# Kernel optimization log

Hardware: AMD Instinct MI355X
Metric: run time of the kernel (lower is better)

Reference implementation:

```python
import jax, jax.numpy as jnp
import numpy as np

# ---- module hyperparameters (match init_kwargs) ----
N_BASIS = 4            # lagrange polynomial order n
SEGMENTS = 32
IN_CHANNELS = 64
LENGTH = 2.0
HALF = 0.5 * LENGTH
W_WIDTH = (N_BASIS - 1) * SEGMENTS + 1  # 97
# Lagrange interpolation nodes on [-HALF, HALF] (uniform, as in high_order_layers_torch LagrangePoly)
_XNODES = np.linspace(-HALF, HALF, N_BASIS).astype(np.float32)


def _lagrange_basis(x):
    """x: [...] -> basis values [..., n]; basis_j(x) = prod_{m!=j} (x-X_m)/(X_j-X_m)."""
    X = jnp.asarray(_XNODES, dtype=x.dtype)
    eye = jnp.eye(N_BASIS, dtype=bool)
    denom = jnp.where(eye, 1.0, X[:, None] - X[None, :])          # [n, n]
    num = x[..., None, None] - X                                   # [..., 1, n] broadcast over j
    terms = jnp.where(eye, 1.0, num / denom)                       # [..., j, m]
    return jnp.prod(terms, axis=-1)                                # [..., n]


def setup_inputs() -> dict:
    key = jax.random.key(0)
    k1, k2 = jax.random.split(key)
    x = jax.random.normal(k1, (32, IN_CHANNELS, 4096), dtype=jnp.float32)
    w = jax.random.uniform(k2, (IN_CHANNELS, W_WIDTH), dtype=jnp.float32,
                           minval=-1.0, maxval=1.0)
    return {"x": x, "w": w}


def reference(x, w):
    B, C, N = x.shape  # [batch, channels, nodes]
    n = N_BASIS

    # bin index with torch-style trunc + clamp
    id_raw = jnp.trunc((x + HALF) / LENGTH * SEGMENTS).astype(jnp.int32)
    id_min = jnp.clip(id_raw, 0, SEGMENTS - 1)                     # [B, C, N]
    id_max = id_min + 1

    wid_min = id_min * (n - 1)                                     # [B, C, N]

    # gather n consecutive weights per element from the shared table
    E = B * C * N
    wrange = wid_min.reshape(-1)[:, None] + jnp.arange(n)          # [E, n]
    # original: windex = (arange(E*n)//n) % in_channels  == (arange(E) % C) per row
    windex = (jnp.arange(E) % C)[:, None]                          # [E, 1]
    wg = w[windex, wrange]                                         # [E, n]
    # original reshape: view(-1, nodes, in_channels, n)
    wv = wg.reshape(B, N, C, n)                                    # [B, N, C, n]

    # rescale x into the local segment coordinate [-HALF, HALF]
    eta = lambda idx: idx.astype(x.dtype) / SEGMENTS * 2.0 - 1.0
    x_min = eta(id_min)
    x_max = eta(id_max)
    x_in = LENGTH * ((x - x_min) / (x_max - x_min)) - HALF         # [B, C, N]

    basis = _lagrange_basis(x_in)                                  # [B, C, N, n]
    # contract basis with gathered weights (note transposed node/channel layout of wv)
    out = jnp.einsum("bcnj,bncj->bcn", basis, wv)                  # [B, C, N]
    return out
```

## Files before the change

### kernel.cpp

```cpp
#include <hip/hip_runtime.h>

#define NCH      64
#define WW       97
#define NTHREADS 512

typedef float        f32x4  __attribute__((ext_vector_type(4)));
typedef float        f32x4u __attribute__((ext_vector_type(4), aligned(4)));
typedef _Float16     h16x4  __attribute__((ext_vector_type(4)));
typedef _Float16     h16x8  __attribute__((ext_vector_type(8)));
typedef unsigned int u32;
typedef unsigned int u32x2 __attribute__((ext_vector_type(2)));

__global__ __launch_bounds__(NTHREADS)
void pw_kernel(const float* __restrict__ x,
               const float* __restrict__ w,
               float* __restrict__ out) {
  __shared__ h16x4 wexp[NCH * 32];
  __shared__ __align__(8) unsigned char sidT[64 * 72];

  const int g   = blockIdx.x;
  const int b   = (g & 7) | ((g >> 9) << 3);
  const int t   = (g >> 3) & 63;
  const int tid = threadIdx.x;

  const float* xrow = x + (((size_t)(b * NCH + t)) << 12);
  const f32x4 r0 = *reinterpret_cast<const f32x4*>(xrow + (tid << 3));
  const f32x4 r1 = *reinterpret_cast<const f32x4*>(xrow + (tid << 3) + 4);

  #pragma unroll
  for (int k = 0; k < 2; ++k) {
    const int pr = tid + k * NTHREADS;
    const int c  = pr >> 4, k2 = pr & 15;
    const float* wr = w + c * WW + 6 * k2;
    const f32x4u wa = *reinterpret_cast<const f32x4u*>(wr);
    const f32x4u wb = *reinterpret_cast<const f32x4u*>(wr + 3);
    h16x8 hh;
    {
      const float A = wa[3] - wa[0], B = wa[3] + wa[0];
      const float C = wa[1] - wa[2], D = wa[1] + wa[2];
      hh[0] = (_Float16)fmaf(D, 0.5625f, B * -0.0625f);
      hh[1] = (_Float16)fmaf(C, -1.6875f, A * -0.0625f);
      hh[2] = (_Float16)((B - D) * 0.5625f);
      hh[3] = (_Float16)fmaf(C, 1.6875f, A * 0.5625f);
    }
    {
      const float A = wb[3] - wb[0], B = wb[3] + wb[0];
      const float C = wb[1] - wb[2], D = wb[1] + wb[2];
      hh[4] = (_Float16)fmaf(D, 0.5625f, B * -0.0625f);
      hh[5] = (_Float16)fmaf(C, -1.6875f, A * -0.0625f);
      hh[6] = (_Float16)((B - D) * 0.5625f);
      hh[7] = (_Float16)fmaf(C, 1.6875f, A * 0.5625f);
    }
    *reinterpret_cast<h16x8*>(&wexp[(c << 5) + (k2 << 1)]) = hh;
  }

  {
    u32 p0 = 0, p1 = 0;
    #pragma unroll
    for (int i = 0; i < 4; ++i) {
      const float t0 = fmaf(r0[i], 16.0f, 16.0f);
      int id0 = (int)t0;
      id0 = id0 < 0 ? 0 : (id0 > 31 ? 31 : id0);
      p0 |= (u32)id0 << (8 * i);
      const float t1 = fmaf(r1[i], 16.0f, 16.0f);
      int id1 = (int)t1;
      id1 = id1 < 0 ? 0 : (id1 > 31 ? 31 : id1);
      p1 |= (u32)id1 << (8 * i);
    }
    u32x2 pv; pv[0] = p0; pv[1] = p1;
    *reinterpret_cast<u32x2*>(&sidT[(tid >> 3) * 72 + ((tid & 7) << 3)]) = pv;
  }
  __syncthreads();

  const int l  = tid & 63;
  const int wv = tid >> 6;
  const int q  = l & 15;
  const int a  = l >> 4;
  const int u0 = q << 2;
  const int c0 = (wv << 3) + (a << 1);

  const int dwo = (c0 >> 2) << 2;
  u32 idw[4];
  #pragma unroll
  for (int i = 0; i < 4; ++i)
    idw[i] = *reinterpret_cast<const u32*>(&sidT[(u0 + i) * 72 + dwo]);
  const int sh0 = (c0 & 3) * 8;

  const size_t obase = (((size_t)(b * NCH + c0)) << 12) + ((size_t)(t << 6)) + u0;

  #pragma unroll
  for (int j = 0; j < 2; ++j) {
    const f32x4 own = *reinterpret_cast<const f32x4*>(x + obase + ((size_t)j << 12));
    const int cb = (c0 + j) << 5;
    const int sh = sh0 + 8 * j;
    f32x4 res;
    #pragma unroll
    for (int i = 0; i < 4; ++i) {
      const float xv = own[i];
      const float tt = fmaf(xv, 16.0f, 16.0f);
      int idm = (int)tt;
      idm = idm < 0 ? 0 : (idm > 31 ? 31 : idm);
      const float xin = fmaf(xv, 32.0f, fmaf((float)idm, -2.0f, 31.0f));

      const int widx = (idw[i] >> sh) & 31;
      const h16x4 hc = wexp[cb + widx];
      res[i] = fmaf(fmaf(fmaf((float)hc[3], xin, (float)hc[2]), xin,
                         (float)hc[1]), xin, (float)hc[0]);
    }
    __builtin_nontemporal_store(res,
        reinterpret_cast<f32x4*>(out + obase + ((size_t)j << 12)));
  }
}

extern "C" void kernel_launch(void* const* d_in, const int* in_sizes, int n_in,
                              void* d_out, int out_size, void* d_ws, size_t ws_size,
                              hipStream_t stream) {
  const float* x = (const float*)d_in[0];
  const float* w = (const float*)d_in[1];
  float* out    = (float*)d_out;
  pw_kernel<<<dim3(2048), NTHREADS, 0, stream>>>(x, w, out);
}
```

Measured before the change: 16.30 us.

## Tile index transpose as cyclic 16^3 cube orbits so x is read once

Each element's output depends on the bin id of a permuted element (c,t,u) -> (t,u,c) index. The old kernel read each x row twice: once to build the transposed id table and again for its own value. The new scheme splits each batch's 64x64x64 index space into 16-cubes grouped by cyclic rotation orbits. Each block stages up to three cubes whose transposes map onto each other, so every loaded x value is reused for both id staging and its own output. This halves global reads of x, at the cost of more complex indexing, uneven work per block (orbits of size 1 vs 3) and fewer blocks (768).

Result: slower. 22.56 us (+38.4%).

```diff
diff --git a/kernel.cpp b/kernel.cpp
--- a/kernel.cpp
+++ b/kernel.cpp
@@ -1,8 +1,7 @@
 #include <hip/hip_runtime.h>
 
-#define NCH      64
-#define WW       97
-#define NTHREADS 512
+#define NCH 64
+#define WW  97
 
 typedef float        f32x4  __attribute__((ext_vector_type(4)));
 typedef float        f32x4u __attribute__((ext_vector_type(4), aligned(4)));
@@ -11,25 +10,41 @@
 typedef unsigned int u32;
 typedef unsigned int u32x2 __attribute__((ext_vector_type(2)));
 
-__global__ __launch_bounds__(NTHREADS)
+__constant__ unsigned char ORBITS[24] = {
+  0x00, 0x15, 0x2A, 0x3F,
+  0x01, 0x02, 0x03, 0x05, 0x0A, 0x0F,
+  0x06, 0x09, 0x07, 0x0D, 0x0B, 0x0E,
+  0x16, 0x17, 0x1A, 0x1F, 0x2B, 0x2F,
+  0x1B, 0x1E
+};
+
+#define TAU_STR 24
+#define RHO_STR 392
+
+__global__ __launch_bounds__(512)
 void pw_kernel(const float* __restrict__ x,
                const float* __restrict__ w,
                float* __restrict__ out) {
   __shared__ h16x4 wexp[NCH * 32];
-  __shared__ __align__(8) unsigned char sidT[64 * 72];
+  __shared__ __align__(8) unsigned char sid[3][16 * RHO_STR];
 
-  const int g   = blockIdx.x;
-  const int b   = (g & 7) | ((g >> 9) << 3);
-  const int t   = (g >> 3) & 63;
+  const int g    = blockIdx.x;
+  const int b    = g & 31;
+  const int o    = g >> 5;
+  const int ob   = ORBITS[o];
+  const int nreg = (o < 4) ? 1 : 3;
+  const int e0   = ((ob >> 4) & 3) << 4;
+  const int e1   = ((ob >> 2) & 3) << 4;
+  const int e2   = (ob & 3) << 4;
+
   const int tid = threadIdx.x;
-
-  const float* xrow = x + (((size_t)(b * NCH + t)) << 12);
-  const f32x4 r0 = *reinterpret_cast<const f32x4*>(xrow + (tid << 3));
-  const f32x4 r1 = *reinterpret_cast<const f32x4*>(xrow + (tid << 3) + 4);
+  const int rho = tid >> 5;
+  const int sig = (tid >> 1) & 15;
+  const int h   = tid & 1;
 
   #pragma unroll
   for (int k = 0; k < 2; ++k) {
-    const int pr = tid + k * NTHREADS;
+    const int pr = tid + k * 512;
     const int c  = pr >> 4, k2 = pr & 15;
     const float* wr = w + c * WW + 6 * k2;
     const f32x4u wa = *reinterpret_cast<const f32x4u*>(wr);
@@ -54,61 +69,71 @@
     *reinterpret_cast<h16x8*>(&wexp[(c << 5) + (k2 << 1)]) = hh;
   }
 
-  {
+  auto stage = [&](int r, int R, int T, int O, f32x4& qa, f32x4& qb) {
+    const float* p = x + (((size_t)(b * NCH + R + rho)) << 12)
+                       + ((T + sig) << 6) + O + 8 * h;
+    qa = *reinterpret_cast<const f32x4*>(p);
+    qb = *reinterpret_cast<const f32x4*>(p + 4);
     u32 p0 = 0, p1 = 0;
     #pragma unroll
     for (int i = 0; i < 4; ++i) {
-      const float t0 = fmaf(r0[i], 16.0f, 16.0f);
+      const float t0 = fmaf(qa[i], 16.0f, 16.0f);
       int id0 = (int)t0;
       id0 = id0 < 0 ? 0 : (id0 > 31 ? 31 : id0);
       p0 |= (u32)id0 << (8 * i);
-      const float t1 = fmaf(r1[i], 16.0f, 16.0f);
+      const float t1 = fmaf(qb[i], 16.0f, 16.0f);
       int id1 = (int)t1;
       id1 = id1 < 0 ? 0 : (id1 > 31 ? 31 : id1);
       p1 |= (u32)id1 << (8 * i);
     }
     u32x2 pv; pv[0] = p0; pv[1] = p1;
-    *reinterpret_cast<u32x2*>(&sidT[(tid >> 3) * 72 + ((tid & 7) << 3)]) = pv;
+    *reinterpret_cast<u32x2*>(&sid[r][rho * RHO_STR + sig * TAU_STR + 8 * h]) = pv;
+  };
+
+  f32x4 v0a, v0b, v1a, v1b, v2a, v2b;
+  stage(0, e0, e1, e2, v0a, v0b);
+  if (nreg == 3) {
+    stage(1, e1, e2, e0, v1a, v1b);
+    stage(2, e2, e0, e1, v2a, v2b);
   }
   __syncthreads();
 
-  const int l  = tid & 63;
-  const int wv = tid >> 6;
-  const int q  = l & 15;
-  const int a  = l >> 4;
-  const int u0 = q << 2;
-  const int c0 = (wv << 3) + (a << 1);
+  auto cube = [&](int CB, int TB, int UB, int m, const f32x4& qa, const f32x4& qb) {
+    const int c  = CB + rho;
+    const int t  = TB + sig;
+    const int u0 = UB + 8 * h;
+    const unsigned char* sp = &sid[m][sig * RHO_STR + 192 * h + (rho & ~3)];
+    u32 d[8];
+    #pragma unroll
+    for (int i = 0; i < 8; ++i)
+      d[i] = *reinterpret_cast<const u32*>(sp + i * TAU_STR);
+    const int sh = (rho & 3) * 8;
+    const int cw = c << 5;
 
-  const int dwo = (c0 >> 2) << 2;
-  u32 idw[4];
-  #pragma unroll
-  for (int i = 0; i < 4; ++i)
-    idw[i] = *reinterpret_cast<const u32*>(&sidT[(u0 + i) * 72 + dwo]);
-  const int sh0 = (c0 & 3) * 8;
-
-  const size_t obase = (((size_t)(b * NCH + c0)) << 12) + ((size_t)(t << 6)) + u0;
-
-  #pragma unroll
-  for (int j = 0; j < 2; ++j) {
-    const f32x4 own = *reinterpret_cast<const f32x4*>(x + obase + ((size_t)j << 12));
-    const int cb = (c0 + j) << 5;
-    const int sh = sh0 + 8 * j;
-    f32x4 res;
+    f32x4 res0, res1;
     #pragma unroll
-    for (int i = 0; i < 4; ++i) {
-      const float xv = own[i];
+    for (int i = 0; i < 8; ++i) {
+      const float xv = (i < 4) ? qa[i & 3] : qb[i & 3];
       const float tt = fmaf(xv, 16.0f, 16.0f);
       int idm = (int)tt;
       idm = idm < 0 ? 0 : (idm > 31 ? 31 : idm);
       const float xin = fmaf(xv, 32.0f, fmaf((float)idm, -2.0f, 31.0f));
 
-      const int widx = (idw[i] >> sh) & 31;
-      const h16x4 hc = wexp[cb + widx];
-      res[i] = fmaf(fmaf(fmaf((float)hc[3], xin, (float)hc[2]), xin,
-                         (float)hc[1]), xin, (float)hc[0]);
+      const int widx = (d[i] >> sh) & 31;
+      const h16x4 hc = wexp[cw + widx];
+      const float r = fmaf(fmaf(fmaf((float)hc[3], xin, (float)hc[2]), xin,
+                                (float)hc[1]), xin, (float)hc[0]);
+      if (i < 4) res0[i & 3] = r; else res1[i & 3] = r;
     }
-    __builtin_nontemporal_store(res,
-        reinterpret_cast<f32x4*>(out + obase + ((size_t)j << 12)));
+    float* op = out + (((size_t)(b * NCH + c)) << 12) + (t << 6) + u0;
+    __builtin_nontemporal_store(res0, reinterpret_cast<f32x4*>(op));
+    __builtin_nontemporal_store(res1, reinterpret_cast<f32x4*>(op + 4));
+  };
+
+  cube(e0, e1, e2, (nreg == 1) ? 0 : 1, v0a, v0b);
+  if (nreg == 3) {
+    cube(e1, e2, e0, 2, v1a, v1b);
+    cube(e2, e0, e1, 0, v2a, v2b);
   }
 }
 
@@ -118,5 +143,5 @@
   const float* x = (const float*)d_in[0];
   const float* w = (const float*)d_in[1];
   float* out    = (float*)d_out;
-  pw_kernel<<<dim3(2048), NTHREADS, 0, stream>>>(x, w, out);
+  pw_kernel<<<dim3(24 * 32), 512, 0, stream>>>(x, w, out);
 }
```
